# Kernel tuning notes

Measured on AMD Instinct MI355X. Metric: run time of the kernel, lower is better.

## Reference

```python
import jax, jax.numpy as jnp
import numpy as np

BAG, SEQ, D = 8, 512, 768      # docs per bag, seq len, bert hidden (d_model)
NB = 4                          # bridge spans kept per doc (subsampling cap regime)
NPD = 2 + NB                    # nodes per doc: h, t, bridges
N = BAG * NPD                   # total entity nodes in the bag graph (48)
T = N * N                       # matrix cells fed to MatTransformer (2304)
H = 8
DK = D // H                     # head dim 96
DFF, L = 1024, 4                # MatTransformer ffn width / num_layers
NREL = 97                       # num_relations (DocRED)
EPS = 1e-5


def _ln(x, g, b):
    m = jnp.mean(x, axis=-1, keepdims=True)
    v = jnp.var(x, axis=-1, keepdims=True)
    return (x - m) * jax.lax.rsqrt(v + EPS) * g + b


def setup_inputs() -> dict:
    key = jax.random.key(0)
    ks = jax.random.split(key, 16)
    s = 0.02
    p = {}
    # stand-in for BERT last hidden states
    p['embedding'] = jax.random.normal(ks[0], (BAG, SEQ, D), jnp.float32)
    # entity spans per doc: [h, t, b1..bNB] x (start, end) inclusive, from get_htb markers
    starts = jax.random.randint(ks[1], (BAG, NPD), 0, SEQ - 9)
    lens = jax.random.randint(ks[2], (BAG, NPD), 1, 9)
    p['spans'] = jnp.stack([starts, starts + lens - 1], axis=-1).astype(jnp.int32)
    # pairwise relation encoders wu / wv / ln1
    p['Wu'] = jax.random.normal(ks[3], (D, D)) * s; p['bu'] = jnp.zeros((D,))
    p['Wv'] = jax.random.normal(ks[4], (D, D)) * s; p['bv'] = jnp.zeros((D,))
    p['Wl'] = jax.random.normal(ks[5], (D, D)) * s; p['bl'] = jnp.zeros((D,))
    # MatTransformer: L layers of MHA + FFN, params stacked over layers
    p['Wq'] = jax.random.normal(ks[6], (L, D, D)) * s;  p['bq'] = jnp.zeros((L, D))
    p['Wk'] = jax.random.normal(ks[7], (L, D, D)) * s;  p['bk'] = jnp.zeros((L, D))
    p['Wvm'] = jax.random.normal(ks[8], (L, D, D)) * s; p['bvm'] = jnp.zeros((L, D))
    p['Wo'] = jax.random.normal(ks[9], (L, D, D)) * s;  p['bo'] = jnp.zeros((L, D))
    p['F1'] = jax.random.normal(ks[10], (L, D, DFF)) * s; p['f1'] = jnp.zeros((L, DFF))
    p['F2'] = jax.random.normal(ks[11], (L, DFF, D)) * s; p['f2'] = jnp.zeros((L, D))
    p['g1'] = jnp.ones((L, D)); p['be1'] = jnp.zeros((L, D))
    p['g2'] = jnp.ones((L, D)); p['be2'] = jnp.zeros((L, D))
    # final norm + predictor
    p['ng'] = jnp.ones((D,)); p['nb'] = jnp.zeros((D,))
    p['Wp'] = jax.random.normal(ks[12], (D, NREL)) * s; p['bp'] = jnp.zeros((NREL,))
    return p


def _forward(embedding, spans, Wu, bu, Wv, bv, Wl, bl, Wq, bq, Wk, bk, Wvm, bvm,
             Wo, bo, F1, f1, F2, f2, g1, be1, g2, be2, ng, nb, Wp, bp):
    # --- ragged span gather + max pooling (masked max, vectorized) ---
    pos = jnp.arange(SEQ)
    m = (pos >= spans[..., :1]) & (pos <= spans[..., 1:])          # [BAG, NPD, SEQ]
    neg = jnp.finfo(embedding.dtype).min
    pooled = jnp.max(jnp.where(m[..., None], embedding[:, None, :, :], neg), axis=2)  # [BAG, NPD, D]
    htb = pooled.reshape(N, D)                                      # h/t/bridge node embs
    # --- pairwise outer-sum relation encoding: relu(ln1(relu(u_i + v_j))) ---
    u = htb @ Wu + bu
    v = htb @ Wv + bv
    rel = jax.nn.relu(jax.nn.relu(u[:, None, :] + v[None, :, :]) @ Wl + bl)  # [N, N, D]
    # --- MatTransformer: multi-head self-attention over the N*N matrix cells ---
    x = rel.reshape(T, D)
    scale = 1.0 / np.sqrt(DK).astype(np.float32)
    for l in range(L):
        q = (x @ Wq[l] + bq[l]).reshape(T, H, DK)
        k = (x @ Wk[l] + bk[l]).reshape(T, H, DK)
        vv = (x @ Wvm[l] + bvm[l]).reshape(T, H, DK)
        att = jax.nn.softmax(jnp.einsum('qhd,khd->hqk', q, k) * scale, axis=-1)
        o = jnp.einsum('hqk,khd->qhd', att, vv).reshape(T, D) @ Wo[l] + bo[l]
        x = _ln(x + o, g1[l], be1[l])
        f = jax.nn.relu(x @ F1[l] + f1[l]) @ F2[l] + f2[l]
        x = _ln(x + f, g2[l], be2[l])
    rel_m = x.reshape(N, N, D)
    # --- gather (h_pos, t_pos) cells: h at i*NPD, t at i*NPD+1 ---
    hp = jnp.arange(BAG) * NPD
    t_feature = rel_m[hp, hp + 1]                                   # [BAG, D]
    ht_logits = _ln(t_feature, ng, nb) @ Wp + bp                    # [BAG, NREL]
    bag_logit = jnp.max(ht_logits, axis=0, keepdims=True)           # [1, NREL]
    return bag_logit, ht_logits


def reference(embedding, spans, Wu, bu, Wv, bv, Wl, bl, Wq, bq, Wk, bk, Wvm, bvm,
              Wo, bo, F1, f1, F2, f2, g1, be1, g2, be2, ng, nb, Wp, bp):
    return _forward(embedding, spans, Wu, bu, Wv, bv, Wl, bl, Wq, bq, Wk, bk,
                    Wvm, bvm, Wo, bo, F1, f1, F2, f2, g1, be1, g2, be2, ng, nb, Wp, bp)
```

## Files before the change

### kernel.cpp

```cpp
#include <hip/hip_runtime.h>
#include <hip/hip_bf16.h>

typedef __hip_bfloat16 bf16;
typedef __bf16 bf16x8 __attribute__((ext_vector_type(8)));
typedef float f32x4 __attribute__((ext_vector_type(4)));

#define BAG 8
#define SEQ 512
#define DM 768
#define NPD 6
#define NNODE 48
#define TT 2304
#define NH 8
#define DKH 96
#define DFF 1024
#define NLAYER 4
#define NREL 97
#define SP 3
#define KSPAN (TT / SP)
#define LN_EPS 1e-5f

__device__ __forceinline__ float b2f(const bf16 x) { return __bfloat162float(x); }
__device__ __forceinline__ bf16 f2b(float f) { return __float2bfloat16(f); }
__device__ __forceinline__ unsigned short f2bu(float f) {
    bf16 h = __float2bfloat16(f);
    return *reinterpret_cast<unsigned short*>(&h);
}

__global__ __launch_bounds__(256) void span_pool(const float* __restrict__ emb,
                                                 const int* __restrict__ spans,
                                                 bf16* __restrict__ htb) {
    const int n = blockIdx.x;
    const int b = n / NPD;
    int s0 = spans[n * 2 + 0];
    int s1 = spans[n * 2 + 1];
    s0 = min(max(s0, 0), SEQ - 1);
    s1 = min(max(s1, s0), SEQ - 1);
    const float* base = emb + (size_t)b * SEQ * DM;
    for (int d = threadIdx.x; d < DM; d += 256) {
        float m = -3.0e38f;
        for (int s = s0; s <= s1; ++s) m = fmaxf(m, base[(size_t)s * DM + d]);
        htb[(size_t)n * DM + d] = f2b(m);
    }
}

__global__ __launch_bounds__(256) void prep_wt3(const float* __restrict__ W0,
                                                const float* __restrict__ W1,
                                                const float* __restrict__ W2,
                                                bf16* __restrict__ Wt) {
    __shared__ __align__(16) __bf16 tile[64][72];
    const int z = blockIdx.z;
    const float* W = (z == 0) ? W0 : (z == 1) ? W1 : W2;
    bf16* out = Wt + (size_t)z * DM * DM;
    const int t = threadIdx.x;
    const int k0 = blockIdx.x * 64, n0 = blockIdx.y * 64;
    const int r = t >> 2, cg = (t & 3) * 16;
#pragma unroll
    for (int i = 0; i < 4; ++i) {
        const float4 v = *(const float4*)&W[(size_t)(k0 + r) * DM + n0 + cg + 4 * i];
        tile[r][cg + 4 * i + 0] = (__bf16)v.x;
        tile[r][cg + 4 * i + 1] = (__bf16)v.y;
        tile[r][cg + 4 * i + 2] = (__bf16)v.z;
        tile[r][cg + 4 * i + 3] = (__bf16)v.w;
    }
    __syncthreads();
#pragma unroll
    for (int i = 0; i < 2; ++i) {
        bf16x8 o;
#pragma unroll
        for (int j = 0; j < 8; ++j) o[j] = tile[cg + 8 * i + j][r];
        *(bf16x8*)&out[(size_t)(n0 + r) * DM + k0 + cg + 8 * i] = o;
    }
}

__global__ __launch_bounds__(256) void prep6(const float* __restrict__ Wq,
                                             const float* __restrict__ Wk,
                                             const float* __restrict__ Wv,
                                             const float* __restrict__ Wo,
                                             const float* __restrict__ F1,
                                             const float* __restrict__ F2,
                                             bf16* __restrict__ slab) {
    __shared__ __align__(16) __bf16 tile[64][72];
    const int z = blockIdx.z;
    int K = DM, N = DM;
    const float* W;
    size_t off;
    switch (z) {
        case 0: W = Wq; off = 0;       break;
        case 1: W = Wk; off = 589824;  break;
        case 2: W = Wv; off = 1179648; break;
        case 3: W = Wo; off = 1769472; break;
        case 4: W = F1; off = 2359296; N = DFF; break;
        default: W = F2; off = 3145728; K = DFF; break;
    }
    const int k0 = blockIdx.x * 64, n0 = blockIdx.y * 64;
    if (k0 >= K || n0 >= N) return;
    bf16* out = slab + off;
    const int t = threadIdx.x;
    const int r = t >> 2, cg = (t & 3) * 16;
#pragma unroll
    for (int i = 0; i < 4; ++i) {
        const float4 v = *(const float4*)&W[(size_t)(k0 + r) * N + n0 + cg + 4 * i];
        tile[r][cg + 4 * i + 0] = (__bf16)v.x;
        tile[r][cg + 4 * i + 1] = (__bf16)v.y;
        tile[r][cg + 4 * i + 2] = (__bf16)v.z;
        tile[r][cg + 4 * i + 3] = (__bf16)v.w;
    }
    __syncthreads();
#pragma unroll
    for (int i = 0; i < 2; ++i) {
        bf16x8 o;
#pragma unroll
        for (int j = 0; j < 8; ++j) o[j] = tile[cg + 8 * i + j][r];
        *(bf16x8*)&out[(size_t)(n0 + r) * K + k0 + cg + 8 * i] = o;
    }
}

template <int RELU>
__global__ __launch_bounds__(128) void gemm_bt64(const bf16* __restrict__ A,
                                                 const bf16* __restrict__ Bt,
                                                 const float* __restrict__ bias,
                                                 bf16* __restrict__ C,
                                                 int M, int N, int K) {
    __shared__ __align__(16) __bf16 As[2][64][72];
    __shared__ __align__(16) __bf16 Bs[2][64][72];
    const int t = threadIdx.x;
    const int w = t >> 6, lane = t & 63;
    const int quad = lane >> 4, l15 = lane & 15;
    const int row0 = blockIdx.y * 64, col0 = blockIdx.x * 64;
    const int s_row = t >> 1, s_off = (t & 1) * 32;
    const bool a_ok = (row0 + s_row) < M;

    const f32x4 fz = {0.f, 0.f, 0.f, 0.f};
    f32x4 acc[2][4];
#pragma unroll
    for (int m = 0; m < 2; ++m)
#pragma unroll
        for (int i = 0; i < 4; ++i) acc[m][i] = fz;

    bf16x8 av[4], bv[4];
#pragma unroll
    for (int j = 0; j < 4; ++j)
#pragma unroll
        for (int e = 0; e < 8; ++e) av[j][e] = (__bf16)0.0f;
    if (a_ok)
#pragma unroll
        for (int j = 0; j < 4; ++j)
            av[j] = *(const bf16x8*)&A[(size_t)(row0 + s_row) * K + s_off + 8 * j];
#pragma unroll
    for (int j = 0; j < 4; ++j)
        bv[j] = *(const bf16x8*)&Bt[(size_t)(col0 + s_row) * K + s_off + 8 * j];

    int cur = 0;
    for (int k0 = 0; k0 < K; k0 += 64) {
#pragma unroll
        for (int j = 0; j < 4; ++j) {
            *(bf16x8*)&As[cur][s_row][s_off + 8 * j] = av[j];
            *(bf16x8*)&Bs[cur][s_row][s_off + 8 * j] = bv[j];
        }
        __syncthreads();

        if (k0 + 64 < K) {
            if (a_ok)
#pragma unroll
                for (int j = 0; j < 4; ++j)
                    av[j] = *(const bf16x8*)&A[(size_t)(row0 + s_row) * K + k0 + 64 + s_off + 8 * j];
#pragma unroll
            for (int j = 0; j < 4; ++j)
                bv[j] = *(const bf16x8*)&Bt[(size_t)(col0 + s_row) * K + k0 + 64 + s_off + 8 * j];
        }

#pragma unroll
        for (int kk = 0; kk < 2; ++kk) {
            const bf16x8 af0 = *(const bf16x8*)&As[cur][32 * w + l15][quad * 8 + 32 * kk];
            const bf16x8 af1 = *(const bf16x8*)&As[cur][32 * w + 16 + l15][quad * 8 + 32 * kk];
#pragma unroll
            for (int nt = 0; nt < 4; ++nt) {
                const bf16x8 bfv = *(const bf16x8*)&Bs[cur][16 * nt + l15][quad * 8 + 32 * kk];
                acc[0][nt] = __builtin_amdgcn_mfma_f32_16x16x32_bf16(af0, bfv, acc[0][nt], 0, 0, 0);
                acc[1][nt] = __builtin_amdgcn_mfma_f32_16x16x32_bf16(af1, bfv, acc[1][nt], 0, 0, 0);
            }
        }
        cur ^= 1;
    }

#pragma unroll
    for (int nt = 0; nt < 4; ++nt) {
        const int col = col0 + 16 * nt + l15;
        const float bvl = bias[col];
#pragma unroll
        for (int m = 0; m < 2; ++m)
#pragma unroll
            for (int r = 0; r < 4; ++r) {
                const int row = row0 + 32 * w + 16 * m + quad * 4 + r;
                if (row < M) {
                    float v = acc[m][nt][r] + bvl;
                    if (RELU) v = fmaxf(v, 0.f);
                    C[(size_t)row * N + col] = f2b(v);
                }
            }
    }
}

__global__ __launch_bounds__(128) void gemm_qkv2(const bf16* __restrict__ A,
                                                 const bf16* __restrict__ Bt,
                                                 const float* __restrict__ b0,
                                                 const float* __restrict__ b1,
                                                 const float* __restrict__ b2,
                                                 bf16* __restrict__ C0,
                                                 bf16* __restrict__ C1,
                                                 bf16* __restrict__ Vt) {
    __shared__ __align__(16) __bf16 As[2][64][72];
    __shared__ __align__(16) __bf16 Bs[2][64][72];
    const int t = threadIdx.x;
    const int w = t >> 6, lane = t & 63;
    const int quad = lane >> 4, l15 = lane & 15;
    const int row0 = blockIdx.y * 64, col0 = blockIdx.x * 64;
    const int s_row = t >> 1, s_off = (t & 1) * 32;

    const f32x4 fz = {0.f, 0.f, 0.f, 0.f};
    f32x4 acc[2][4];
#pragma unroll
    for (int m = 0; m < 2; ++m)
#pragma unroll
        for (int i = 0; i < 4; ++i) acc[m][i] = fz;

    bf16x8 av[4], bv[4];
#pragma unroll
    for (int j = 0; j < 4; ++j) {
        av[j] = *(const bf16x8*)&A[(size_t)(row0 + s_row) * DM + s_off + 8 * j];
        bv[j] = *(const bf16x8*)&Bt[(size_t)(col0 + s_row) * DM + s_off + 8 * j];
    }

    int cur = 0;
    for (int k0 = 0; k0 < DM; k0 += 64) {
#pragma unroll
        for (int j = 0; j < 4; ++j) {
            *(bf16x8*)&As[cur][s_row][s_off + 8 * j] = av[j];
            *(bf16x8*)&Bs[cur][s_row][s_off + 8 * j] = bv[j];
        }
        __syncthreads();

        if (k0 + 64 < DM) {
#pragma unroll
            for (int j = 0; j < 4; ++j) {
                av[j] = *(const bf16x8*)&A[(size_t)(row0 + s_row) * DM + k0 + 64 + s_off + 8 * j];
                bv[j] = *(const bf16x8*)&Bt[(size_t)(col0 + s_row) * DM + k0 + 64 + s_off + 8 * j];
            }
        }

#pragma unroll
        for (int kk = 0; kk < 2; ++kk) {
            const bf16x8 af0 = *(const bf16x8*)&As[cur][32 * w + l15][quad * 8 + 32 * kk];
            const bf16x8 af1 = *(const bf16x8*)&As[cur][32 * w + 16 + l15][quad * 8 + 32 * kk];
#pragma unroll
            for (int nt = 0; nt < 4; ++nt) {
                const bf16x8 bfv = *(const bf16x8*)&Bs[cur][16 * nt + l15][quad * 8 + 32 * kk];
                acc[0][nt] = __builtin_amdgcn_mfma_f32_16x16x32_bf16(af0, bfv, acc[0][nt], 0, 0, 0);
                acc[1][nt] = __builtin_amdgcn_mfma_f32_16x16x32_bf16(af1, bfv, acc[1][nt], 0, 0, 0);
            }
        }
        cur ^= 1;
    }

    const int buf = col0 / DM;
    const int lc0 = col0 - buf * DM;
    if (buf < 2) {
        bf16* Cb = (buf == 0) ? C0 : C1;
        const float* bb = (buf == 0) ? b0 : b1;
#pragma unroll
        for (int nt = 0; nt < 4; ++nt) {
            const int col = lc0 + 16 * nt + l15;
            const float bvl = bb[col];
#pragma unroll
            for (int m = 0; m < 2; ++m)
#pragma unroll
                for (int r = 0; r < 4; ++r) {
                    const int row = row0 + 32 * w + 16 * m + quad * 4 + r;
                    Cb[(size_t)row * DM + col] = f2b(acc[m][nt][r] + bvl);
                }
        }
    } else {
        __bf16 (*Tb)[72] = As[0];
        __syncthreads();
#pragma unroll
        for (int nt = 0; nt < 4; ++nt) {
            const float bvl = b2[lc0 + 16 * nt + l15];
#pragma unroll
            for (int m = 0; m < 2; ++m)
#pragma unroll
                for (int r = 0; r < 4; ++r)
                    Tb[16 * nt + l15][32 * w + 16 * m + quad * 4 + r] = (__bf16)(acc[m][nt][r] + bvl);
        }
        __syncthreads();
        const int c = t >> 1, half = (t & 1) * 32;
#pragma unroll
        for (int j = 0; j < 4; ++j)
            *(bf16x8*)&Vt[(size_t)(lc0 + c) * TT + row0 + half + 8 * j] =
                *(const bf16x8*)&Tb[c][half + 8 * j];
    }
}

template <int RELU>
__global__ __launch_bounds__(128) void gemm_mfma(const bf16* __restrict__ A,
                                                 const float* __restrict__ W,
                                                 const float* __restrict__ bias,
                                                 bf16* __restrict__ C,
                                                 int M, int N, int K) {
    __shared__ __align__(16) __bf16 As[32][40];
    __shared__ __align__(16) __bf16 Bs[64][40];
    const int t = threadIdx.x;
    const int w = t >> 6, lane = t & 63;
    const int quad = lane >> 4, l15 = lane & 15;
    const int row0 = blockIdx.y * 32, col0 = blockIdx.x * 64;
    const int s_row = t >> 2, s_kg = (t & 3) * 8;
    const int s_colg = (t & 15) * 4, s_kp = t >> 4;
    const bool a_ok = (row0 + s_row) < M;
    const f32x4 fz = {0.f, 0.f, 0.f, 0.f};
    f32x4 acc[4];
#pragma unroll
    for (int i = 0; i < 4; ++i) acc[i] = fz;

    for (int k0 = 0; k0 < K; k0 += 32) {
        bf16x8 av;
        for (int j = 0; j < 8; ++j) av[j] = (__bf16)0.0f;
        if (a_ok) av = *(const bf16x8*)&A[(size_t)(row0 + s_row) * K + k0 + s_kg];
        *(bf16x8*)&As[s_row][s_kg] = av;
#pragma unroll
        for (int rep = 0; rep < 2; ++rep) {
            const int kp = s_kp + 8 * rep;
            const size_t gb = (size_t)(k0 + 2 * kp) * N + col0 + s_colg;
            const float4 w0 = *(const float4*)&W[gb];
            const float4 w1 = *(const float4*)&W[gb + N];
#pragma unroll
            for (int i = 0; i < 4; ++i) {
                ushort2 pk;
                pk.x = f2bu((&w0.x)[i]);
                pk.y = f2bu((&w1.x)[i]);
                *(ushort2*)&Bs[s_colg + i][2 * kp] = pk;
            }
        }
        __syncthreads();
        const bf16x8 af = *(const bf16x8*)&As[16 * w + l15][quad * 8];
#pragma unroll
        for (int nt = 0; nt < 4; ++nt) {
            const bf16x8 bfv = *(const bf16x8*)&Bs[16 * nt + l15][quad * 8];
            acc[nt] = __builtin_amdgcn_mfma_f32_16x16x32_bf16(af, bfv, acc[nt], 0, 0, 0);
        }
        __syncthreads();
    }
#pragma unroll
    for (int nt = 0; nt < 4; ++nt) {
        const int col = col0 + 16 * nt + l15;
        const float bvl = bias[col];
#pragma unroll
        for (int r = 0; r < 4; ++r) {
            const int row = row0 + 16 * w + quad * 4 + r;
            if (row < M) {
                float v = acc[nt][r] + bvl;
                if (RELU) v = fmaxf(v, 0.f);
                C[(size_t)row * N + col] = f2b(v);
            }
        }
    }
}

__global__ __launch_bounds__(256) void build_relA(const bf16* __restrict__ u,
                                                  const bf16* __restrict__ v,
                                                  bf16* __restrict__ A) {
    const int cell = blockIdx.x;
    const int i = cell / NNODE, j = cell % NNODE;
    for (int k = threadIdx.x; k < DM; k += 256) {
        A[(size_t)cell * DM + k] = f2b(fmaxf(b2f(u[i * DM + k]) + b2f(v[j * DM + k]), 0.f));
    }
}

__global__ __launch_bounds__(256) void transpose_v(const bf16* __restrict__ v,
                                                   bf16* __restrict__ vt) {
    __shared__ __align__(16) __bf16 tile[64][72];
    const int t = threadIdx.x;
    const int bx = blockIdx.x, by = blockIdx.y;
    const int r = t >> 2, cg = (t & 3) * 16;
#pragma unroll
    for (int i = 0; i < 2; ++i)
        *(bf16x8*)&tile[r][cg + 8 * i] =
            *(const bf16x8*)&v[(size_t)(by * 64 + r) * DM + bx * 64 + cg + 8 * i];
    __syncthreads();
#pragma unroll
    for (int i = 0; i < 2; ++i) {
        bf16x8 o;
#pragma unroll
        for (int j = 0; j < 8; ++j) o[j] = tile[cg + 8 * i + j][r];
        *(bf16x8*)&vt[(size_t)(bx * 64 + r) * TT + by * 64 + cg + 8 * i] = o;
    }
}

template <int MODE>
__global__ __launch_bounds__(256) void attn_mfma(const bf16* __restrict__ qb,
                                                 const bf16* __restrict__ kb,
                                                 const bf16* __restrict__ vtb,
                                                 bf16* __restrict__ ob,
                                                 bf16* __restrict__ Opb,
                                                 float* __restrict__ Lp,
                                                 int kspan) {
    __shared__ __align__(16) __bf16 Ks[64][104];
    __shared__ __align__(16) __bf16 Vts[96][72];
    __shared__ __align__(16) __bf16 Ps[4][16][72];

    const int t = threadIdx.x;
    const int w = t >> 6, lane = t & 63;
    const int quad = lane >> 4, l15 = lane & 15;
    const int h = blockIdx.y;
    const int q0 = blockIdx.x * 64;
    const int p = blockIdx.z;
    const int kstart = p * kspan;
    const float scale = 0.10206207261596575f;

    bf16x8 qf[3];
#pragma unroll
    for (int ks = 0; ks < 3; ++ks) {
        qf[ks] = *(const bf16x8*)&qb[(size_t)(q0 + 16 * w + l15) * DM + h * DKH + quad * 8 + 32 * ks];
#pragma unroll
        for (int j = 0; j < 8; ++j) qf[ks][j] = (__bf16)((float)qf[ks][j] * scale);
    }

    const f32x4 fz = {0.f, 0.f, 0.f, 0.f};
    f32x4 Oa[6];
#pragma unroll
    for (int i = 0; i < 6; ++i) Oa[i] = fz;
    float lrow[4] = {0.f, 0.f, 0.f, 0.f};

    bf16x8 kreg[3], vreg[3];
#pragma unroll
    for (int i = 0; i < 3; ++i) {
        const int idx = t + 256 * i;
        const int r = idx / 12, c = idx % 12;
        kreg[i] = *(const bf16x8*)&kb[(size_t)(kstart + r) * DM + h * DKH + c * 8];
        const int d = idx >> 3, ck = idx & 7;
        vreg[i] = *(const bf16x8*)&vtb[(size_t)(h * DKH + d) * TT + kstart + ck * 8];
    }

    for (int kc = kstart; kc < kstart + kspan; kc += 64) {
        __syncthreads();
#pragma unroll
        for (int i = 0; i < 3; ++i) {
            const int idx = t + 256 * i;
            const int r = idx / 12, c = idx % 12;
            *(bf16x8*)&Ks[r][c * 8] = kreg[i];
            const int d = idx >> 3, ck = idx & 7;
            *(bf16x8*)&Vts[d][ck * 8] = vreg[i];
        }
        __syncthreads();

        if (kc + 64 < kstart + kspan) {
#pragma unroll
            for (int i = 0; i < 3; ++i) {
                const int idx = t + 256 * i;
                const int r = idx / 12, c = idx % 12;
                kreg[i] = *(const bf16x8*)&kb[(size_t)(kc + 64 + r) * DM + h * DKH + c * 8];
                const int d = idx >> 3, ck = idx & 7;
                vreg[i] = *(const bf16x8*)&vtb[(size_t)(h * DKH + d) * TT + kc + 64 + ck * 8];
            }
        }

        f32x4 Sa[4] = {fz, fz, fz, fz};
#pragma unroll
        for (int nt = 0; nt < 4; ++nt)
#pragma unroll
            for (int ks = 0; ks < 3; ++ks) {
                const bf16x8 kf = *(const bf16x8*)&Ks[l15 + 16 * nt][quad * 8 + 32 * ks];
                Sa[nt] = __builtin_amdgcn_mfma_f32_16x16x32_bf16(qf[ks], kf, Sa[nt], 0, 0, 0);
            }

#pragma unroll
        for (int r = 0; r < 4; ++r) {
            const float p0 = __expf(Sa[0][r]), p1 = __expf(Sa[1][r]);
            const float p2 = __expf(Sa[2][r]), p3 = __expf(Sa[3][r]);
            Ps[w][quad * 4 + r][l15]      = (__bf16)p0;
            Ps[w][quad * 4 + r][l15 + 16] = (__bf16)p1;
            Ps[w][quad * 4 + r][l15 + 32] = (__bf16)p2;
            Ps[w][quad * 4 + r][l15 + 48] = (__bf16)p3;
            float ps = p0 + p1 + p2 + p3;
            ps += __shfl_xor(ps, 1);
            ps += __shfl_xor(ps, 2);
            ps += __shfl_xor(ps, 4);
            ps += __shfl_xor(ps, 8);
            lrow[r] += ps;
        }

        const bf16x8 pa0 = *(const bf16x8*)&Ps[w][l15][quad * 8];
        const bf16x8 pa1 = *(const bf16x8*)&Ps[w][l15][32 + quad * 8];

#pragma unroll
        for (int nt = 0; nt < 6; ++nt) {
            const bf16x8 vf0 = *(const bf16x8*)&Vts[l15 + 16 * nt][quad * 8];
            const bf16x8 vf1 = *(const bf16x8*)&Vts[l15 + 16 * nt][32 + quad * 8];
            Oa[nt] = __builtin_amdgcn_mfma_f32_16x16x32_bf16(pa0, vf0, Oa[nt], 0, 0, 0);
            Oa[nt] = __builtin_amdgcn_mfma_f32_16x16x32_bf16(pa1, vf1, Oa[nt], 0, 0, 0);
        }
    }

    if (MODE == 0) {
#pragma unroll
        for (int nt = 0; nt < 6; ++nt)
#pragma unroll
            for (int r = 0; r < 4; ++r) {
                const int row = q0 + 16 * w + quad * 4 + r;
                ob[(size_t)row * DM + h * DKH + 16 * nt + l15] = f2b(Oa[nt][r] / lrow[r]);
            }
    } else {
#pragma unroll
        for (int nt = 0; nt < 6; ++nt)
#pragma unroll
            for (int r = 0; r < 4; ++r) {
                const int row = q0 + 16 * w + quad * 4 + r;
                Opb[((size_t)p * TT + row) * DM + h * DKH + 16 * nt + l15] = f2b(Oa[nt][r]);
            }
        if (l15 == 0) {
#pragma unroll
            for (int r = 0; r < 4; ++r) {
                const int row = q0 + 16 * w + quad * 4 + r;
                Lp[((size_t)p * NH + h) * TT + row] = lrow[r];
            }
        }
    }
}

__global__ __launch_bounds__(256) void attn_merge(const bf16* __restrict__ Opb,
                                                  const float* __restrict__ Lp,
                                                  bf16* __restrict__ ob) {
    __shared__ float Ls[8][NH];
    const int r0 = blockIdx.x * 8;
    const int t = threadIdx.x;
    if (t < 8 * NH) {
        const int rl = t >> 3, hh = t & 7;
        float L = 0.f;
#pragma unroll
        for (int p = 0; p < SP; ++p) L += Lp[((size_t)p * NH + hh) * TT + r0 + rl];
        Ls[rl][hh] = 1.0f / L;
    }
    __syncthreads();
    const int rl = t >> 5, lane = t & 31;
    const int row = r0 + rl;
#pragma unroll
    for (int j = 0; j < 3; ++j) {
        const int d0 = lane * 8 + j * 256;
        float acc[8];
#pragma unroll
        for (int e = 0; e < 8; ++e) acc[e] = 0.f;
#pragma unroll
        for (int p = 0; p < SP; ++p) {
            const bf16x8 vv = *(const bf16x8*)&Opb[((size_t)p * TT + row) * DM + d0];
#pragma unroll
            for (int e = 0; e < 8; ++e) acc[e] += (float)vv[e];
        }
        const float s = Ls[rl][d0 / DKH];
        bf16x8 o;
#pragma unroll
        for (int e = 0; e < 8; ++e) o[e] = (__bf16)(acc[e] * s);
        *(bf16x8*)&ob[(size_t)row * DM + d0] = o;
    }
}

__global__ __launch_bounds__(256) void add_ln(bf16* __restrict__ x,
                                              const bf16* __restrict__ r,
                                              const float* __restrict__ g,
                                              const float* __restrict__ be) {
    __shared__ float red[4];
    const int row = blockIdx.x;
    bf16* xr = x + (size_t)row * DM;
    const bf16* rr = r + (size_t)row * DM;
    const int t = threadIdx.x;

    float v0 = b2f(xr[t]) + b2f(rr[t]);
    float v1 = b2f(xr[t + 256]) + b2f(rr[t + 256]);
    float v2 = b2f(xr[t + 512]) + b2f(rr[t + 512]);
    float s = v0 + v1 + v2;
#pragma unroll
    for (int off = 32; off >= 1; off >>= 1) s += __shfl_xor(s, off);
    if ((t & 63) == 0) red[t >> 6] = s;
    __syncthreads();
    s = red[0] + red[1] + red[2] + red[3];
    const float mean = s * (1.f / 768.f);
    __syncthreads();

    const float d0 = v0 - mean, d1 = v1 - mean, d2 = v2 - mean;
    float ss = d0 * d0 + d1 * d1 + d2 * d2;
#pragma unroll
    for (int off = 32; off >= 1; off >>= 1) ss += __shfl_xor(ss, off);
    if ((t & 63) == 0) red[t >> 6] = ss;
    __syncthreads();
    ss = red[0] + red[1] + red[2] + red[3];
    const float inv = rsqrtf(ss * (1.f / 768.f) + LN_EPS);

    xr[t]       = f2b(d0 * inv * g[t]       + be[t]);
    xr[t + 256] = f2b(d1 * inv * g[t + 256] + be[t + 256]);
    xr[t + 512] = f2b(d2 * inv * g[t + 512] + be[t + 512]);
}

__global__ __launch_bounds__(256) void predict(const bf16* __restrict__ x,
                                               const float* __restrict__ ng,
                                               const float* __restrict__ nb,
                                               const float* __restrict__ Wp,
                                               const float* __restrict__ bp,
                                               float* __restrict__ out) {
    __shared__ float xs[BAG][DM];
    __shared__ float red[4][BAG];
    const int t = threadIdx.x;
    const int rel = blockIdx.x;
    const int wid = t >> 6, lane = t & 63;

    for (int rep = 0; rep < 2; ++rep) {
        const int b = wid + rep * 4;
        const bf16* row = x + (size_t)(294 * b + 1) * DM;
        float vals[12];
        float s = 0.f;
#pragma unroll
        for (int i = 0; i < 12; ++i) { vals[i] = b2f(row[lane + i * 64]); s += vals[i]; }
#pragma unroll
        for (int off = 32; off >= 1; off >>= 1) s += __shfl_xor(s, off);
        const float mean = s * (1.f / 768.f);
        float ss = 0.f;
#pragma unroll
        for (int i = 0; i < 12; ++i) { const float d = vals[i] - mean; ss += d * d; }
#pragma unroll
        for (int off = 32; off >= 1; off >>= 1) ss += __shfl_xor(ss, off);
        const float inv = rsqrtf(ss * (1.f / 768.f) + LN_EPS);
#pragma unroll
        for (int i = 0; i < 12; ++i) {
            const int d = lane + i * 64;
            xs[b][d] = (vals[i] - mean) * inv * ng[d] + nb[d];
        }
    }
    __syncthreads();

    float pb[BAG];
#pragma unroll
    for (int b = 0; b < BAG; ++b) pb[b] = 0.f;
    for (int k = t; k < DM; k += 256) {
        const float wv = Wp[(size_t)k * NREL + rel];
#pragma unroll
        for (int b = 0; b < BAG; ++b) pb[b] += xs[b][k] * wv;
    }
#pragma unroll
    for (int b = 0; b < BAG; ++b)
#pragma unroll
        for (int off = 32; off >= 1; off >>= 1) pb[b] += __shfl_xor(pb[b], off);
    if (lane == 0)
#pragma unroll
        for (int b = 0; b < BAG; ++b) red[wid][b] = pb[b];
    __syncthreads();
    if (t == 0) {
        float mx = -3.0e38f;
        for (int b = 0; b < BAG; ++b) {
            const float v = red[0][b] + red[1][b] + red[2][b] + red[3][b] + bp[rel];
            out[NREL + b * NREL + rel] = v;
            mx = fmaxf(mx, v);
        }
        out[rel] = mx;
    }
}

extern "C" void kernel_launch(void* const* d_in, const int* in_sizes, int n_in,
                              void* d_out, int out_size, void* d_ws, size_t ws_size,
                              hipStream_t stream) {
    const float* emb  = (const float*)d_in[0];
    const int* spans  = (const int*)d_in[1];
    const float* Wu = (const float*)d_in[2];  const float* bu = (const float*)d_in[3];
    const float* Wv = (const float*)d_in[4];  const float* bv = (const float*)d_in[5];
    const float* Wl = (const float*)d_in[6];  const float* bl = (const float*)d_in[7];
    const float* Wq = (const float*)d_in[8];  const float* bq = (const float*)d_in[9];
    const float* Wk = (const float*)d_in[10]; const float* bk = (const float*)d_in[11];
    const float* Wvm = (const float*)d_in[12]; const float* bvm = (const float*)d_in[13];
    const float* Wo = (const float*)d_in[14]; const float* bo = (const float*)d_in[15];
    const float* F1 = (const float*)d_in[16]; const float* f1 = (const float*)d_in[17];
    const float* F2 = (const float*)d_in[18]; const float* f2 = (const float*)d_in[19];
    const float* g1 = (const float*)d_in[20]; const float* be1 = (const float*)d_in[21];
    const float* g2 = (const float*)d_in[22]; const float* be2 = (const float*)d_in[23];
    const float* ng = (const float*)d_in[24]; const float* nb = (const float*)d_in[25];
    const float* Wp = (const float*)d_in[26]; const float* bp = (const float*)d_in[27];

    char* wsb = (char*)d_ws;
    bf16* htb = (bf16*)(wsb + 0);
    bf16* ub  = (bf16*)(wsb + 73728);
    bf16* vbn = (bf16*)(wsb + 147456);
    bf16* x   = (bf16*)(wsb + 221184);
    bf16* Bq  = (bf16*)(wsb + 3760128);
    bf16* Bk  = (bf16*)(wsb + 7299072);
    bf16* Bv  = (bf16*)(wsb + 10838016);
    bf16* Vt  = (bf16*)(wsb + 15556608);
    bf16* slab = (bf16*)(wsb + 19095552);
    bf16* Opb = (bf16*)(wsb + 26959872);
    float* Lp = (float*)(wsb + 48193536);

    const size_t FULL_END = 48635904;
    const bool use_full = ws_size >= FULL_END;

    span_pool<<<NNODE, 256, 0, stream>>>(emb, spans, htb);

    if (use_full) {
        prep_wt3<<<dim3(12, 12, 3), 256, 0, stream>>>(Wu, Wv, Wl, slab);
        gemm_bt64<0><<<dim3(12, 1), 128, 0, stream>>>(htb, slab, bu, ub, NNODE, DM, DM);
        gemm_bt64<0><<<dim3(12, 1), 128, 0, stream>>>(htb, slab + 589824, bv, vbn, NNODE, DM, DM);
        build_relA<<<TT, 256, 0, stream>>>(ub, vbn, Bq);
        gemm_bt64<1><<<dim3(12, TT / 64), 128, 0, stream>>>(Bq, slab + 1179648, bl, x, TT, DM, DM);

        for (int l = 0; l < NLAYER; ++l) {
            const size_t wo = (size_t)l * DM * DM;
            const size_t f1o = (size_t)l * DM * DFF;
            prep6<<<dim3(16, 16, 6), 256, 0, stream>>>(Wq + wo, Wk + wo, Wvm + wo,
                                                       Wo + wo, F1 + f1o, F2 + f1o, slab);
            gemm_qkv2<<<dim3(36, TT / 64), 128, 0, stream>>>(x, slab, bq + l * DM, bk + l * DM,
                                                             bvm + l * DM, Bq, Bk, Vt);
            attn_mfma<1><<<dim3(TT / 64, NH, SP), 256, 0, stream>>>(Bq, Bk, Vt, Bq, Opb, Lp, KSPAN);
            attn_merge<<<TT / 8, 256, 0, stream>>>(Opb, Lp, Bq);
            gemm_bt64<0><<<dim3(12, TT / 64), 128, 0, stream>>>(Bq, slab + 1769472, bo + l * DM, Bk, TT, DM, DM);
            add_ln<<<TT, 256, 0, stream>>>(x, Bk, g1 + l * DM, be1 + l * DM);
            gemm_bt64<1><<<dim3(16, TT / 64), 128, 0, stream>>>(x, slab + 2359296, f1 + l * DFF, Bv, TT, DFF, DM);
            gemm_bt64<0><<<dim3(12, TT / 64), 128, 0, stream>>>(Bv, slab + 3145728, f2 + l * DM, Bk, TT, DM, DFF);
            add_ln<<<TT, 256, 0, stream>>>(x, Bk, g2 + l * DM, be2 + l * DM);
        }
    } else {
        gemm_mfma<0><<<dim3(12, 2), 128, 0, stream>>>(htb, Wu, bu, ub, NNODE, DM, DM);
        gemm_mfma<0><<<dim3(12, 2), 128, 0, stream>>>(htb, Wv, bv, vbn, NNODE, DM, DM);
        build_relA<<<TT, 256, 0, stream>>>(ub, vbn, Bq);
        gemm_mfma<1><<<dim3(12, TT / 32), 128, 0, stream>>>(Bq, Wl, bl, x, TT, DM, DM);

        for (int l = 0; l < NLAYER; ++l) {
            const size_t wo = (size_t)l * DM * DM;
            const size_t f1o = (size_t)l * DM * DFF;
            gemm_mfma<0><<<dim3(12, TT / 32), 128, 0, stream>>>(x, Wq + wo, bq + l * DM, Bq, TT, DM, DM);
            gemm_mfma<0><<<dim3(12, TT / 32), 128, 0, stream>>>(x, Wk + wo, bk + l * DM, Bk, TT, DM, DM);
            gemm_mfma<0><<<dim3(12, TT / 32), 128, 0, stream>>>(x, Wvm + wo, bvm + l * DM, Bv, TT, DM, DM);
            transpose_v<<<dim3(DM / 64, TT / 64), 256, 0, stream>>>(Bv, Vt);
            attn_mfma<0><<<dim3(TT / 64, NH, 1), 256, 0, stream>>>(Bq, Bk, Vt, Bq, Opb, Lp, TT);
            gemm_mfma<0><<<dim3(12, TT / 32), 128, 0, stream>>>(Bq, Wo + wo, bo + l * DM, Bk, TT, DM, DM);
            add_ln<<<TT, 256, 0, stream>>>(x, Bk, g1 + l * DM, be1 + l * DM);
            gemm_mfma<1><<<dim3(16, TT / 32), 128, 0, stream>>>(x, F1 + f1o, f1 + l * DFF, Bv, TT, DFF, DM);
            gemm_mfma<0><<<dim3(12, TT / 32), 128, 0, stream>>>(Bv, F2 + f1o, f2 + l * DM, Bk, TT, DM, DFF);
            add_ln<<<TT, 256, 0, stream>>>(x, Bk, g2 + l * DM, be2 + l * DM);
        }
    }

    predict<<<NREL, 256, 0, stream>>>(x, ng, nb, Wp, bp, (float*)d_out);
}
```

Measured before the change: 749.2 us.

## Use four-wave 2x2 GEMM tiles, merge Wu/Wv GEMMs, double attention splits

Changes the 64x64 GEMM kernels from two waves to four waves per block, with each wave computing a 32x32 subtile in a 2x2 layout. This lowers accumulator count per wave and raises the wave count per tile, aiming for better latency hiding. The Wu and Wv projections are fused into one GEMM with a dual bias, writing an interleaved buffer, and build_relA gains a stride argument to read it. The attention key split count goes from 3 to 6, which adds parallelism but costs more partial outputs and more merge work.

```diff
diff --git a/kernel.cpp b/kernel.cpp
--- a/kernel.cpp
+++ b/kernel.cpp
@@ -16,7 +16,7 @@
 #define DFF 1024
 #define NLAYER 4
 #define NREL 97
-#define SP 3
+#define SP 6
 #define KSPAN (TT / SP)
 #define LN_EPS 1e-5f
 
@@ -116,45 +116,47 @@
     }
 }
 
-template <int RELU>
-__global__ __launch_bounds__(128) void gemm_bt64(const bf16* __restrict__ A,
-                                                 const bf16* __restrict__ Bt,
-                                                 const float* __restrict__ bias,
-                                                 bf16* __restrict__ C,
-                                                 int M, int N, int K) {
+template <int RELU, int DUAL>
+__global__ __launch_bounds__(256) void gemm_bt256(const bf16* __restrict__ A,
+                                                  const bf16* __restrict__ Bt,
+                                                  const float* __restrict__ bias,
+                                                  const float* __restrict__ bias2,
+                                                  bf16* __restrict__ C,
+                                                  int M, int N, int K) {
     __shared__ __align__(16) __bf16 As[2][64][72];
     __shared__ __align__(16) __bf16 Bs[2][64][72];
     const int t = threadIdx.x;
     const int w = t >> 6, lane = t & 63;
     const int quad = lane >> 4, l15 = lane & 15;
+    const int wr = w >> 1, wc = w & 1;
     const int row0 = blockIdx.y * 64, col0 = blockIdx.x * 64;
-    const int s_row = t >> 1, s_off = (t & 1) * 32;
+    const int s_row = t >> 2, s_off = (t & 3) * 16;
     const bool a_ok = (row0 + s_row) < M;
 
     const f32x4 fz = {0.f, 0.f, 0.f, 0.f};
-    f32x4 acc[2][4];
+    f32x4 acc[2][2];
 #pragma unroll
     for (int m = 0; m < 2; ++m)
 #pragma unroll
-        for (int i = 0; i < 4; ++i) acc[m][i] = fz;
-
-    bf16x8 av[4], bv[4];
-#pragma unroll
-    for (int j = 0; j < 4; ++j)
+        for (int n = 0; n < 2; ++n) acc[m][n] = fz;
+
+    bf16x8 av[2], bv[2];
+#pragma unroll
+    for (int j = 0; j < 2; ++j)
 #pragma unroll
         for (int e = 0; e < 8; ++e) av[j][e] = (__bf16)0.0f;
     if (a_ok)
 #pragma unroll
-        for (int j = 0; j < 4; ++j)
+        for (int j = 0; j < 2; ++j)
             av[j] = *(const bf16x8*)&A[(size_t)(row0 + s_row) * K + s_off + 8 * j];
 #pragma unroll
-    for (int j = 0; j < 4; ++j)
+    for (int j = 0; j < 2; ++j)
         bv[j] = *(const bf16x8*)&Bt[(size_t)(col0 + s_row) * K + s_off + 8 * j];
 
     int cur = 0;
     for (int k0 = 0; k0 < K; k0 += 64) {
 #pragma unroll
-        for (int j = 0; j < 4; ++j) {
+        for (int j = 0; j < 2; ++j) {
             *(bf16x8*)&As[cur][s_row][s_off + 8 * j] = av[j];
             *(bf16x8*)&Bs[cur][s_row][s_off + 8 * j] = bv[j];
         }
@@ -163,38 +165,38 @@
         if (k0 + 64 < K) {
             if (a_ok)
 #pragma unroll
-                for (int j = 0; j < 4; ++j)
+                for (int j = 0; j < 2; ++j)
                     av[j] = *(const bf16x8*)&A[(size_t)(row0 + s_row) * K + k0 + 64 + s_off + 8 * j];
 #pragma unroll
-            for (int j = 0; j < 4; ++j)
+            for (int j = 0; j < 2; ++j)
                 bv[j] = *(const bf16x8*)&Bt[(size_t)(col0 + s_row) * K + k0 + 64 + s_off + 8 * j];
         }
 
 #pragma unroll
         for (int kk = 0; kk < 2; ++kk) {
-            const bf16x8 af0 = *(const bf16x8*)&As[cur][32 * w + l15][quad * 8 + 32 * kk];
-            const bf16x8 af1 = *(const bf16x8*)&As[cur][32 * w + 16 + l15][quad * 8 + 32 * kk];
-#pragma unroll
-            for (int nt = 0; nt < 4; ++nt) {
-                const bf16x8 bfv = *(const bf16x8*)&Bs[cur][16 * nt + l15][quad * 8 + 32 * kk];
-                acc[0][nt] = __builtin_amdgcn_mfma_f32_16x16x32_bf16(af0, bfv, acc[0][nt], 0, 0, 0);
-                acc[1][nt] = __builtin_amdgcn_mfma_f32_16x16x32_bf16(af1, bfv, acc[1][nt], 0, 0, 0);
-            }
+            const bf16x8 af0 = *(const bf16x8*)&As[cur][wr * 32 + l15][quad * 8 + 32 * kk];
+            const bf16x8 af1 = *(const bf16x8*)&As[cur][wr * 32 + 16 + l15][quad * 8 + 32 * kk];
+            const bf16x8 bf0 = *(const bf16x8*)&Bs[cur][wc * 32 + l15][quad * 8 + 32 * kk];
+            const bf16x8 bf1 = *(const bf16x8*)&Bs[cur][wc * 32 + 16 + l15][quad * 8 + 32 * kk];
+            acc[0][0] = __builtin_amdgcn_mfma_f32_16x16x32_bf16(af0, bf0, acc[0][0], 0, 0, 0);
+            acc[0][1] = __builtin_amdgcn_mfma_f32_16x16x32_bf16(af0, bf1, acc[0][1], 0, 0, 0);
+            acc[1][0] = __builtin_amdgcn_mfma_f32_16x16x32_bf16(af1, bf0, acc[1][0], 0, 0, 0);
+            acc[1][1] = __builtin_amdgcn_mfma_f32_16x16x32_bf16(af1, bf1, acc[1][1], 0, 0, 0);
         }
         cur ^= 1;
     }
 
 #pragma unroll
-    for (int nt = 0; nt < 4; ++nt) {
-        const int col = col0 + 16 * nt + l15;
-        const float bvl = bias[col];
+    for (int n = 0; n < 2; ++n) {
+        const int col = col0 + wc * 32 + 16 * n + l15;
+        const float bvl = (DUAL && col >= DM) ? bias2[col - DM] : bias[col];
 #pragma unroll
         for (int m = 0; m < 2; ++m)
 #pragma unroll
             for (int r = 0; r < 4; ++r) {
-                const int row = row0 + 32 * w + 16 * m + quad * 4 + r;
+                const int row = row0 + wr * 32 + 16 * m + quad * 4 + r;
                 if (row < M) {
-                    float v = acc[m][nt][r] + bvl;
+                    float v = acc[m][n][r] + bvl;
                     if (RELU) v = fmaxf(v, 0.f);
                     C[(size_t)row * N + col] = f2b(v);
                 }
@@ -202,32 +204,33 @@
     }
 }
 
-__global__ __launch_bounds__(128) void gemm_qkv2(const bf16* __restrict__ A,
-                                                 const bf16* __restrict__ Bt,
-                                                 const float* __restrict__ b0,
-                                                 const float* __restrict__ b1,
-                                                 const float* __restrict__ b2,
-                                                 bf16* __restrict__ C0,
-                                                 bf16* __restrict__ C1,
-                                                 bf16* __restrict__ Vt) {
+__global__ __launch_bounds__(256) void gemm_qkv256(const bf16* __restrict__ A,
+                                                   const bf16* __restrict__ Bt,
+                                                   const float* __restrict__ b0,
+                                                   const float* __restrict__ b1,
+                                                   const float* __restrict__ b2,
+                                                   bf16* __restrict__ C0,
+                                                   bf16* __restrict__ C1,
+                                                   bf16* __restrict__ Vt) {
     __shared__ __align__(16) __bf16 As[2][64][72];
     __shared__ __align__(16) __bf16 Bs[2][64][72];
     const int t = threadIdx.x;
     const int w = t >> 6, lane = t & 63;
     const int quad = lane >> 4, l15 = lane & 15;
+    const int wr = w >> 1, wc = w & 1;
     const int row0 = blockIdx.y * 64, col0 = blockIdx.x * 64;
-    const int s_row = t >> 1, s_off = (t & 1) * 32;
+    const int s_row = t >> 2, s_off = (t & 3) * 16;
 
     const f32x4 fz = {0.f, 0.f, 0.f, 0.f};
-    f32x4 acc[2][4];
+    f32x4 acc[2][2];
 #pragma unroll
     for (int m = 0; m < 2; ++m)
 #pragma unroll
-        for (int i = 0; i < 4; ++i) acc[m][i] = fz;
-
-    bf16x8 av[4], bv[4];
-#pragma unroll
-    for (int j = 0; j < 4; ++j) {
+        for (int n = 0; n < 2; ++n) acc[m][n] = fz;
+
+    bf16x8 av[2], bv[2];
+#pragma unroll
+    for (int j = 0; j < 2; ++j) {
         av[j] = *(const bf16x8*)&A[(size_t)(row0 + s_row) * DM + s_off + 8 * j];
         bv[j] = *(const bf16x8*)&Bt[(size_t)(col0 + s_row) * DM + s_off + 8 * j];
     }
@@ -235,7 +238,7 @@
     int cur = 0;
     for (int k0 = 0; k0 < DM; k0 += 64) {
 #pragma unroll
-        for (int j = 0; j < 4; ++j) {
+        for (int j = 0; j < 2; ++j) {
             *(bf16x8*)&As[cur][s_row][s_off + 8 * j] = av[j];
             *(bf16x8*)&Bs[cur][s_row][s_off + 8 * j] = bv[j];
         }
@@ -243,7 +246,7 @@
 
         if (k0 + 64 < DM) {
 #pragma unroll
-            for (int j = 0; j < 4; ++j) {
+            for (int j = 0; j < 2; ++j) {
                 av[j] = *(const bf16x8*)&A[(size_t)(row0 + s_row) * DM + k0 + 64 + s_off + 8 * j];
                 bv[j] = *(const bf16x8*)&Bt[(size_t)(col0 + s_row) * DM + k0 + 64 + s_off + 8 * j];
             }
@@ -251,14 +254,14 @@
 
 #pragma unroll
         for (int kk = 0; kk < 2; ++kk) {
-            const bf16x8 af0 = *(const bf16x8*)&As[cur][32 * w + l15][quad * 8 + 32 * kk];
-            const bf16x8 af1 = *(const bf16x8*)&As[cur][32 * w + 16 + l15][quad * 8 + 32 * kk];
-#pragma unroll
-            for (int nt = 0; nt < 4; ++nt) {
-                const bf16x8 bfv = *(const bf16x8*)&Bs[cur][16 * nt + l15][quad * 8 + 32 * kk];
-                acc[0][nt] = __builtin_amdgcn_mfma_f32_16x16x32_bf16(af0, bfv, acc[0][nt], 0, 0, 0);
-                acc[1][nt] = __builtin_amdgcn_mfma_f32_16x16x32_bf16(af1, bfv, acc[1][nt], 0, 0, 0);
-            }
+            const bf16x8 af0 = *(const bf16x8*)&As[cur][wr * 32 + l15][quad * 8 + 32 * kk];
+            const bf16x8 af1 = *(const bf16x8*)&As[cur][wr * 32 + 16 + l15][quad * 8 + 32 * kk];
+            const bf16x8 bf0 = *(const bf16x8*)&Bs[cur][wc * 32 + l15][quad * 8 + 32 * kk];
+            const bf16x8 bf1 = *(const bf16x8*)&Bs[cur][wc * 32 + 16 + l15][quad * 8 + 32 * kk];
+            acc[0][0] = __builtin_amdgcn_mfma_f32_16x16x32_bf16(af0, bf0, acc[0][0], 0, 0, 0);
+            acc[0][1] = __builtin_amdgcn_mfma_f32_16x16x32_bf16(af0, bf1, acc[0][1], 0, 0, 0);
+            acc[1][0] = __builtin_amdgcn_mfma_f32_16x16x32_bf16(af1, bf0, acc[1][0], 0, 0, 0);
+            acc[1][1] = __builtin_amdgcn_mfma_f32_16x16x32_bf16(af1, bf1, acc[1][1], 0, 0, 0);
         }
         cur ^= 1;
     }
@@ -269,35 +272,36 @@
         bf16* Cb = (buf == 0) ? C0 : C1;
         const float* bb = (buf == 0) ? b0 : b1;
 #pragma unroll
-        for (int nt = 0; nt < 4; ++nt) {
-            const int col = lc0 + 16 * nt + l15;
+        for (int n = 0; n < 2; ++n) {
+            const int col = lc0 + wc * 32 + 16 * n + l15;
             const float bvl = bb[col];
 #pragma unroll
             for (int m = 0; m < 2; ++m)
 #pragma unroll
                 for (int r = 0; r < 4; ++r) {
-                    const int row = row0 + 32 * w + 16 * m + quad * 4 + r;
-                    Cb[(size_t)row * DM + col] = f2b(acc[m][nt][r] + bvl);
+                    const int row = row0 + wr * 32 + 16 * m + quad * 4 + r;
+                    Cb[(size_t)row * DM + col] = f2b(acc[m][n][r] + bvl);
                 }
         }
     } else {
         __bf16 (*Tb)[72] = As[0];
         __syncthreads();
 #pragma unroll
-        for (int nt = 0; nt < 4; ++nt) {
-            const float bvl = b2[lc0 + 16 * nt + l15];
+        for (int n = 0; n < 2; ++n) {
+            const int cl = wc * 32 + 16 * n + l15;
+            const float bvl = b2[lc0 + cl];
 #pragma unroll
             for (int m = 0; m < 2; ++m)
 #pragma unroll
                 for (int r = 0; r < 4; ++r)
-                    Tb[16 * nt + l15][32 * w + 16 * m + quad * 4 + r] = (__bf16)(acc[m][nt][r] + bvl);
+                    Tb[cl][wr * 32 + 16 * m + quad * 4 + r] = (__bf16)(acc[m][n][r] + bvl);
         }
         __syncthreads();
-        const int c = t >> 1, half = (t & 1) * 32;
-#pragma unroll
-        for (int j = 0; j < 4; ++j)
-            *(bf16x8*)&Vt[(size_t)(lc0 + c) * TT + row0 + half + 8 * j] =
-                *(const bf16x8*)&Tb[c][half + 8 * j];
+        const int c = t >> 2, seg = (t & 3) * 16;
+        const bf16x8 o0 = *(const bf16x8*)&Tb[c][seg];
+        const bf16x8 o1 = *(const bf16x8*)&Tb[c][seg + 8];
+        *(bf16x8*)&Vt[(size_t)(lc0 + c) * TT + row0 + seg] = o0;
+        *(bf16x8*)&Vt[(size_t)(lc0 + c) * TT + row0 + seg + 8] = o1;
     }
 }
 
@@ -367,11 +371,13 @@
 
 __global__ __launch_bounds__(256) void build_relA(const bf16* __restrict__ u,
                                                   const bf16* __restrict__ v,
+                                                  int stride,
                                                   bf16* __restrict__ A) {
     const int cell = blockIdx.x;
     const int i = cell / NNODE, j = cell % NNODE;
     for (int k = threadIdx.x; k < DM; k += 256) {
-        A[(size_t)cell * DM + k] = f2b(fmaxf(b2f(u[i * DM + k]) + b2f(v[j * DM + k]), 0.f));
+        A[(size_t)cell * DM + k] =
+            f2b(fmaxf(b2f(u[(size_t)i * stride + k]) + b2f(v[(size_t)j * stride + k]), 0.f));
     }
 }
 
@@ -682,6 +688,7 @@
 
     char* wsb = (char*)d_ws;
     bf16* htb = (bf16*)(wsb + 0);
+    bf16* u2  = (bf16*)(wsb + 73728);
     bf16* ub  = (bf16*)(wsb + 73728);
     bf16* vbn = (bf16*)(wsb + 147456);
     bf16* x   = (bf16*)(wsb + 221184);
@@ -700,30 +707,34 @@
 
     if (use_full) {
         prep_wt3<<<dim3(12, 12, 3), 256, 0, stream>>>(Wu, Wv, Wl, slab);
-        gemm_bt64<0><<<dim3(12, 1), 128, 0, stream>>>(htb, slab, bu, ub, NNODE, DM, DM);
-        gemm_bt64<0><<<dim3(12, 1), 128, 0, stream>>>(htb, slab + 589824, bv, vbn, NNODE, DM, DM);
-        build_relA<<<TT, 256, 0, stream>>>(ub, vbn, Bq);
-        gemm_bt64<1><<<dim3(12, TT / 64), 128, 0, stream>>>(Bq, slab + 1179648, bl, x, TT, DM, DM);
+        gemm_bt256<0, 1><<<dim3(24, 1), 256, 0, stream>>>(htb, slab, bu, bv, u2,
+                                                          NNODE, 2 * DM, DM);
+        build_relA<<<TT, 256, 0, stream>>>(u2, u2 + DM, 2 * DM, Bq);
+        gemm_bt256<1, 0><<<dim3(12, TT / 64), 256, 0, stream>>>(Bq, slab + 1179648, bl, bl, x,
+                                                                TT, DM, DM);
 
         for (int l = 0; l < NLAYER; ++l) {
             const size_t wo = (size_t)l * DM * DM;
             const size_t f1o = (size_t)l * DM * DFF;
             prep6<<<dim3(16, 16, 6), 256, 0, stream>>>(Wq + wo, Wk + wo, Wvm + wo,
                                                        Wo + wo, F1 + f1o, F2 + f1o, slab);
-            gemm_qkv2<<<dim3(36, TT / 64), 128, 0, stream>>>(x, slab, bq + l * DM, bk + l * DM,
-                                                             bvm + l * DM, Bq, Bk, Vt);
+            gemm_qkv256<<<dim3(36, TT / 64), 256, 0, stream>>>(x, slab, bq + l * DM, bk + l * DM,
+                                                               bvm + l * DM, Bq, Bk, Vt);
             attn_mfma<1><<<dim3(TT / 64, NH, SP), 256, 0, stream>>>(Bq, Bk, Vt, Bq, Opb, Lp, KSPAN);
             attn_merge<<<TT / 8, 256, 0, stream>>>(Opb, Lp, Bq);
-            gemm_bt64<0><<<dim3(12, TT / 64), 128, 0, stream>>>(Bq, slab + 1769472, bo + l * DM, Bk, TT, DM, DM);
+            gemm_bt256<0, 0><<<dim3(12, TT / 64), 256, 0, stream>>>(Bq, slab + 1769472, bo + l * DM,
+                                                                    bo + l * DM, Bk, TT, DM, DM);
             add_ln<<<TT, 256, 0, stream>>>(x, Bk, g1 + l * DM, be1 + l * DM);
-            gemm_bt64<1><<<dim3(16, TT / 64), 128, 0, stream>>>(x, slab + 2359296, f1 + l * DFF, Bv, TT, DFF, DM);
-            gemm_bt64<0><<<dim3(12, TT / 64), 128, 0, stream>>>(Bv, slab + 3145728, f2 + l * DM, Bk, TT, DM, DFF);
+            gemm_bt256<1, 0><<<dim3(16, TT / 64), 256, 0, stream>>>(x, slab + 2359296, f1 + l * DFF,
+                                                                    f1 + l * DFF, Bv, TT, DFF, DM);
+            gemm_bt256<0, 0><<<dim3(12, TT / 64), 256, 0, stream>>>(Bv, slab + 3145728, f2 + l * DM,
+                                                                    f2 + l * DM, Bk, TT, DM, DFF);
             add_ln<<<TT, 256, 0, stream>>>(x, Bk, g2 + l * DM, be2 + l * DM);
         }
     } else {
         gemm_mfma<0><<<dim3(12, 2), 128, 0, stream>>>(htb, Wu, bu, ub, NNODE, DM, DM);
         gemm_mfma<0><<<dim3(12, 2), 128, 0, stream>>>(htb, Wv, bv, vbn, NNODE, DM, DM);
-        build_relA<<<TT, 256, 0, stream>>>(ub, vbn, Bq);
+        build_relA<<<TT, 256, 0, stream>>>(ub, vbn, DM, Bq);
         gemm_mfma<1><<<dim3(12, TT / 32), 128, 0, stream>>>(Bq, Wl, bl, x, TT, DM, DM);
 
         for (int l = 0; l < NLAYER; ++l) {
```

Result: faster. 659.6 us (-12.0%).
